# Kernel tuning notes

Measured on AMD Instinct MI355X. Metric: run time of the kernel, lower is better.

Reference implementation:

```python
import jax, jax.numpy as jnp
import numpy as np

N_IN = 4096      # input features
N_NPB = 64       # neurons (inputs) per branch column
N_B = 64         # branches
N_NEXT_H = 256   # next hidden width
COLS = N_B * N_NEXT_H
BATCH = 128


def setup_inputs() -> dict:
    key = jax.random.key(0)
    k1, k2, k3 = jax.random.split(key, 3)
    x = jax.random.normal(k1, (BATCH, N_IN), dtype=jnp.float32)
    # torch kaiming_normal_ on (n_npb, cols): fan_in = cols, gain = sqrt(2)
    std = np.sqrt(2.0 / COLS).astype(np.float32)
    w = jax.random.normal(k2, (N_NPB, COLS), dtype=jnp.float32) * std
    # random per-column input indices (the module's all_branch_indices)
    idx = jax.random.randint(k3, (N_NPB, COLS), 0, N_IN, dtype=jnp.int32)
    return {"x": x, "w": w, "idx": idx}


def _last_write_mask(idx):
    # (row, col) targets. keep[k, c] is True iff no k' > k has idx[k', c] == idx[k, c].
    eq = idx[:, None, :] == idx[None, :, :]                    # [K, K, C]
    later = jnp.triu(jnp.ones((N_NPB, N_NPB), bool), 1)        # k' > k
    return ~jnp.any(eq & later[:, :, None], axis=1)            # [K, C]


def reference(x, w, idx):
    keep = _last_write_mask(idx)
    w_eff = jnp.where(keep, w, jnp.zeros((), x.dtype))         # [K, C]
    cols = jnp.broadcast_to(jnp.arange(COLS), (N_NPB, COLS))
    # scatter weights into dense [n_in, cols] (equals torch's clone+index_put)
    dense = jnp.zeros((N_IN, COLS), x.dtype).at[idx, cols].add(w_eff)
    out = x @ dense                                            # [B, COLS]
    return out.reshape(-1, N_B, N_NEXT_H)
```

## Files before the change

kernel.cpp:

```cpp
#include <hip/hip_runtime.h>

#define N_IN   4096
#define N_NPB  64
#define COLS   16384
#define BATCH  128

typedef unsigned int       uint;
typedef unsigned short     ushort;
typedef unsigned long long u64;
typedef __attribute__((ext_vector_type(2))) _Float16 h2;


template <int KBASE>
static __device__ __forceinline__ uint compute_bits(const int* __restrict__ ip) {
  int v[64 - KBASE];
#pragma unroll
  for (int k = 0; k < 64 - KBASE; ++k) v[k] = ip[(KBASE + k) * COLS];
  uint bits = 0;
#pragma unroll
  for (int j = 0; j < 16; ++j) {
    uint m = 0xffffffffu;
#pragma unroll
    for (int kp = j + 1; kp < 64 - KBASE; ++kp)
      m = min(m, (uint)(v[j] ^ v[kp]));
    bits |= (m != 0u) ? (1u << j) : 0u;
  }
  return bits;
}

__global__ __launch_bounds__(256, 4) void prep_kernel(
    const float* __restrict__ x, const int* __restrict__ idx,
    ushort* __restrict__ xTh, ushort* __restrict__ keep16) {
  const int bid = blockIdx.x;
  const int tid = threadIdx.x;
  if (bid < 512) {
    __shared__ float tile[32][33];
    const int i0 = (bid & 127) * 32;
    const int b0 = (bid >> 7) * 32;
    const int tx = tid & 31;
    const int ty = tid >> 5;
#pragma unroll
    for (int j = 0; j < 32; j += 8)
      tile[ty + j][tx] = x[(b0 + ty + j) * N_IN + i0 + tx];
    __syncthreads();
#pragma unroll
    for (int j = 0; j < 32; j += 8)
      xTh[(i0 + ty + j) * BATCH + b0 + tx] =
          __builtin_bit_cast(ushort, (_Float16)tile[tx][ty + j]);
  } else {
    const int kg = __builtin_amdgcn_readfirstlane(tid >> 6);
    const int c  = (bid - 512) * 64 + (tid & 63);
    const int* ip = idx + c;
    uint bits;
    if      (kg == 0) bits = compute_bits<0>(ip);
    else if (kg == 1) bits = compute_bits<16>(ip);
    else if (kg == 2) bits = compute_bits<32>(ip);
    else              bits = compute_bits<48>(ip);
    keep16[c * 4 + kg] = (ushort)bits;
  }
}

__global__ __launch_bounds__(256, 8) void branch_main_kernel(
    const float* __restrict__ w, const int* __restrict__ idx,
    const u64* __restrict__ keep, const ushort* __restrict__ xTh,
    float* __restrict__ out) {
  __shared__ u64   pk[N_NPB][16];
  __shared__ float res2[16][129];

  const int tid = threadIdx.x;
  const int c0  = blockIdx.x * 16;

  {
    const int cl = tid & 15;
    const int k0 = (tid >> 4) * 4;
    const u64 km = keep[c0 + cl];
#pragma unroll
    for (int p = 0; p < 4; ++p) {
      const int k   = k0 + p;
      const int row = idx[k * COLS + c0 + cl];
      float wv      = w[k * COLS + c0 + cl];
      wv = ((km >> k) & 1ull) ? wv : 0.0f;
      const uint hb = (uint)__builtin_bit_cast(ushort, (_Float16)wv);
      pk[k][cl] = ((u64)((hb << 16) | hb) << 32) | ((u64)((uint)row << 8));
    }
  }
  __syncthreads();

  const int wave = tid >> 6;
  const int lane = tid & 63;
  const int g    = lane >> 4;
  const int b8   = lane & 15;
  const int cl   = wave * 4 + g;

  h2 a0 = (h2)0.0f, a1 = (h2)0.0f, a2 = (h2)0.0f, a3 = (h2)0.0f;
  const char* xb = (const char*)xTh;
  const uint  bo = (uint)b8 * 16;

#pragma unroll
  for (int k = 0; k < N_NPB; ++k) {
    const u64  e   = pk[k][cl];
    const uint off = (uint)e;
    const h2   wh  = __builtin_bit_cast(h2, (uint)(e >> 32));
    const uint4 u  = *(const uint4*)(xb + off + bo);
    a0 += __builtin_bit_cast(h2, u.x) * wh;
    a1 += __builtin_bit_cast(h2, u.y) * wh;
    a2 += __builtin_bit_cast(h2, u.z) * wh;
    a3 += __builtin_bit_cast(h2, u.w) * wh;
  }

  {
    float* r = &res2[cl][b8 * 8];
    r[0] = (float)a0.x; r[1] = (float)a0.y;
    r[2] = (float)a1.x; r[3] = (float)a1.y;
    r[4] = (float)a2.x; r[5] = (float)a2.y;
    r[6] = (float)a3.x; r[7] = (float)a3.y;
  }
  __syncthreads();

  for (int e = tid; e < BATCH * 16; e += 256) {
    const int b = e >> 4, cc = e & 15;
    out[b * COLS + c0 + cc] = res2[cc][b];
  }
}

extern "C" void kernel_launch(void* const* d_in, const int* in_sizes, int n_in,
                              void* d_out, int out_size, void* d_ws, size_t ws_size,
                              hipStream_t stream) {
  const float* x   = (const float*)d_in[0];
  const float* w   = (const float*)d_in[1];
  const int*   idx = (const int*)d_in[2];
  float* out = (float*)d_out;

  char* ws = (char*)d_ws;
  ushort* xTh    = (ushort*)(ws);
  ushort* keep16 = (ushort*)(ws + (1u << 20));
  u64*    keep   = (u64*)(ws + (1u << 20));

  hipLaunchKernelGGL(prep_kernel, dim3(512 + COLS / 64), dim3(256), 0, stream,
                     x, idx, xTh, keep16);
  hipLaunchKernelGGL(branch_main_kernel, dim3(COLS / 16), dim3(256), 0, stream,
                     w, idx, keep, xTh, out);
}
```

Baseline: 23.91 us.

## Stage batch slices of transposed x in LDS and gather per column from shared memory

The prep kernel now computes the last-write mask with a streaming scan over later indices and writes a packed 32-bit (row, fp16 weight) entry per element. x is stored transposed in 8-batch slabs. The main kernel gives each block one 8-batch slab, loaded into 64KB of LDS with global_load_lds, and each thread holds its column's 64 packed entries in registers. Random row gathers therefore hit LDS instead of global/L2, and outputs are written directly without a shared-memory transpose. In exchange, idx is re-read by every batch slab, register pressure rises from 64 packed values per thread, and the large LDS footprint limits occupancy.

```diff
diff --git a/kernel.cpp b/kernel.cpp
--- a/kernel.cpp
+++ b/kernel.cpp
@@ -7,30 +7,43 @@
 
 typedef unsigned int       uint;
 typedef unsigned short     ushort;
-typedef unsigned long long u64;
 typedef __attribute__((ext_vector_type(2))) _Float16 h2;
 
 
-template <int KBASE>
-static __device__ __forceinline__ uint compute_bits(const int* __restrict__ ip) {
-  int v[64 - KBASE];
+static __device__ __forceinline__ ushort f16bits(float v) {
+  return __builtin_bit_cast(ushort, (_Float16)v);
+}
+
+template <int KB>
+static __device__ __forceinline__ void keep_pk(
+    const int* __restrict__ ip, const float* __restrict__ wp,
+    uint* __restrict__ pkout) {
+  int  g[16];
+  uint m[16];
 #pragma unroll
-  for (int k = 0; k < 64 - KBASE; ++k) v[k] = ip[(KBASE + k) * COLS];
-  uint bits = 0;
+  for (int j = 0; j < 16; ++j) { g[j] = ip[(KB + j) * COLS]; m[j] = 0xffffffffu; }
+#pragma unroll
+  for (int j = 0; j < 16; ++j)
+#pragma unroll
+    for (int kp = j + 1; kp < 16; ++kp)
+      m[j] = min(m[j], (uint)(g[j] ^ g[kp]));
+#pragma unroll 4
+  for (int kp = KB + 16; kp < 64; ++kp) {
+    const int vk = ip[kp * COLS];
+#pragma unroll
+    for (int j = 0; j < 16; ++j) m[j] = min(m[j], (uint)(g[j] ^ vk));
+  }
 #pragma unroll
   for (int j = 0; j < 16; ++j) {
-    uint m = 0xffffffffu;
-#pragma unroll
-    for (int kp = j + 1; kp < 64 - KBASE; ++kp)
-      m = min(m, (uint)(v[j] ^ v[kp]));
-    bits |= (m != 0u) ? (1u << j) : 0u;
+    const float wv = (m[j] != 0u) ? wp[(KB + j) * COLS] : 0.0f;
+    pkout[(KB + j) * COLS] = ((uint)g[j] << 16) | (uint)f16bits(wv);
   }
-  return bits;
 }
 
 __global__ __launch_bounds__(256, 4) void prep_kernel(
     const float* __restrict__ x, const int* __restrict__ idx,
-    ushort* __restrict__ xTh, ushort* __restrict__ keep16) {
+    const float* __restrict__ w, ushort* __restrict__ xT16,
+    uint* __restrict__ pku) {
   const int bid = blockIdx.x;
   const int tid = threadIdx.x;
   if (bid < 512) {
@@ -44,83 +57,69 @@
       tile[ty + j][tx] = x[(b0 + ty + j) * N_IN + i0 + tx];
     __syncthreads();
 #pragma unroll
-    for (int j = 0; j < 32; j += 8)
-      xTh[(i0 + ty + j) * BATCH + b0 + tx] =
-          __builtin_bit_cast(ushort, (_Float16)tile[tx][ty + j]);
+    for (int j = 0; j < 32; j += 8) {
+      const int b = b0 + tx, i = i0 + ty + j;
+      xT16[((b >> 3) << 15) + (i << 3) + (b & 7)] = f16bits(tile[tx][ty + j]);
+    }
   } else {
     const int kg = __builtin_amdgcn_readfirstlane(tid >> 6);
     const int c  = (bid - 512) * 64 + (tid & 63);
-    const int* ip = idx + c;
-    uint bits;
-    if      (kg == 0) bits = compute_bits<0>(ip);
-    else if (kg == 1) bits = compute_bits<16>(ip);
-    else if (kg == 2) bits = compute_bits<32>(ip);
-    else              bits = compute_bits<48>(ip);
-    keep16[c * 4 + kg] = (ushort)bits;
+    if      (kg == 0) keep_pk<0 >(idx + c, w + c, pku + c);
+    else if (kg == 1) keep_pk<16>(idx + c, w + c, pku + c);
+    else if (kg == 2) keep_pk<32>(idx + c, w + c, pku + c);
+    else              keep_pk<48>(idx + c, w + c, pku + c);
   }
 }
 
-__global__ __launch_bounds__(256, 8) void branch_main_kernel(
-    const float* __restrict__ w, const int* __restrict__ idx,
-    const u64* __restrict__ keep, const ushort* __restrict__ xTh,
+__global__ __launch_bounds__(512, 4) void gather_kernel(
+    const uint* __restrict__ pku, const ushort* __restrict__ xT16,
     float* __restrict__ out) {
-  __shared__ u64   pk[N_NPB][16];
-  __shared__ float res2[16][129];
+  __shared__ __align__(16) ushort xls[4096 * 8];
 
-  const int tid = threadIdx.x;
-  const int c0  = blockIdx.x * 16;
+  const int tid  = threadIdx.x;
+  const int bid  = blockIdx.x;
+  const int r    = bid & 31;
+  const int s    = bid >> 5;
+  const int wave = tid >> 6;
+  const int lane = tid & 63;
+  const int c    = r * 512 + wave * 64 + lane;
+
+  uint pk[64];
+#pragma unroll
+  for (int k = 0; k < 64; ++k) pk[k] = pku[k * COLS + c];
 
   {
-    const int cl = tid & 15;
-    const int k0 = (tid >> 4) * 4;
-    const u64 km = keep[c0 + cl];
+    const ushort* src = xT16 + (s << 15);
 #pragma unroll
-    for (int p = 0; p < 4; ++p) {
-      const int k   = k0 + p;
-      const int row = idx[k * COLS + c0 + cl];
-      float wv      = w[k * COLS + c0 + cl];
-      wv = ((km >> k) & 1ull) ? wv : 0.0f;
-      const uint hb = (uint)__builtin_bit_cast(ushort, (_Float16)wv);
-      pk[k][cl] = ((u64)((hb << 16) | hb) << 32) | ((u64)((uint)row << 8));
+    for (int t = 0; t < 8; ++t) {
+      const int off = (wave * 8 + t) * 512;
+      __builtin_amdgcn_global_load_lds(
+          (const __attribute__((address_space(1))) void*)(src + off + lane * 8),
+          (__attribute__((address_space(3))) void*)(xls + off), 16, 0, 0);
     }
   }
   __syncthreads();
 
-  const int wave = tid >> 6;
-  const int lane = tid & 63;
-  const int g    = lane >> 4;
-  const int b8   = lane & 15;
-  const int cl   = wave * 4 + g;
-
   h2 a0 = (h2)0.0f, a1 = (h2)0.0f, a2 = (h2)0.0f, a3 = (h2)0.0f;
-  const char* xb = (const char*)xTh;
-  const uint  bo = (uint)b8 * 16;
-
+  const char* xb = (const char*)xls;
 #pragma unroll
-  for (int k = 0; k < N_NPB; ++k) {
-    const u64  e   = pk[k][cl];
-    const uint off = (uint)e;
-    const h2   wh  = __builtin_bit_cast(h2, (uint)(e >> 32));
-    const uint4 u  = *(const uint4*)(xb + off + bo);
+  for (int k = 0; k < 64; ++k) {
+    const uint e   = pk[k];
+    const uint off = (e >> 16) << 4;
+    const uint wb  = e & 0xffffu;
+    const h2   wh  = __builtin_bit_cast(h2, (wb << 16) | wb);
+    const uint4 u  = *(const uint4*)(xb + off);
     a0 += __builtin_bit_cast(h2, u.x) * wh;
     a1 += __builtin_bit_cast(h2, u.y) * wh;
     a2 += __builtin_bit_cast(h2, u.z) * wh;
     a3 += __builtin_bit_cast(h2, u.w) * wh;
   }
 
-  {
-    float* r = &res2[cl][b8 * 8];
-    r[0] = (float)a0.x; r[1] = (float)a0.y;
-    r[2] = (float)a1.x; r[3] = (float)a1.y;
-    r[4] = (float)a2.x; r[5] = (float)a2.y;
-    r[6] = (float)a3.x; r[7] = (float)a3.y;
-  }
-  __syncthreads();
-
-  for (int e = tid; e < BATCH * 16; e += 256) {
-    const int b = e >> 4, cc = e & 15;
-    out[b * COLS + c0 + cc] = res2[cc][b];
-  }
+  float o[8] = {(float)a0.x, (float)a0.y, (float)a1.x, (float)a1.y,
+                (float)a2.x, (float)a2.y, (float)a3.x, (float)a3.y};
+#pragma unroll
+  for (int b = 0; b < 8; ++b)
+    out[(s * 8 + b) * COLS + c] = o[b];
 }
 
 extern "C" void kernel_launch(void* const* d_in, const int* in_sizes, int n_in,
@@ -132,12 +131,11 @@
   float* out = (float*)d_out;
 
   char* ws = (char*)d_ws;
-  ushort* xTh    = (ushort*)(ws);
-  ushort* keep16 = (ushort*)(ws + (1u << 20));
-  u64*    keep   = (u64*)(ws + (1u << 20));
+  ushort* xT16 = (ushort*)(ws);
+  uint*   pku  = (uint*)(ws + (1u << 20));
 
-  hipLaunchKernelGGL(prep_kernel, dim3(512 + COLS / 64), dim3(256), 0, stream,
-                     x, idx, xTh, keep16);
-  hipLaunchKernelGGL(branch_main_kernel, dim3(COLS / 16), dim3(256), 0, stream,
-                     w, idx, keep, xTh, out);
+  hipLaunchKernelGGL(prep_kernel, dim3(768), dim3(256), 0, stream,
+                     x, idx, w, xT16, pku);
+  hipLaunchKernelGGL(gather_kernel, dim3(512), dim3(512), 0, stream,
+                     pku, xT16, out);
 }
```

Measured after the change: 26.19 us. +9.5%, slower.
